# Optimization experiments

Measured on AMD Instinct MI355X. Metric: run time of the kernel, lower is better.

The kernel has to match this reference:

```python
import jax, jax.numpy as jnp
import numpy as np

NUM_HEADS = 16
ROPE_THETA = 1000.0


def _rope(x, cos, sin):
    # x: [B, H, T, d_k]; cos/sin: [T, d_k//2]
    xp = x.reshape(x.shape[:-1] + (x.shape[-1] // 2, 2))
    xe, xo = xp[..., 0], xp[..., 1]
    c = cos[None, None, :, :]
    s = sin[None, None, :, :]
    re = xe * c - xo * s
    ro = xe * s + xo * c
    return jnp.stack((re, ro), axis=-1).reshape(x.shape)


def setup_inputs() -> dict:
    key = jax.random.key(0)
    ks = jax.random.split(key, 5)
    B, T, D = 2, 2048, 1024
    std = 2.0 / (D + D)
    return {
        "x": jax.random.normal(ks[0], (B, T, D), dtype=jnp.float32),
        "wq": jax.random.normal(ks[1], (D, D), dtype=jnp.float32) * std,
        "wk": jax.random.normal(ks[2], (D, D), dtype=jnp.float32) * std,
        "wv": jax.random.normal(ks[3], (D, D), dtype=jnp.float32) * std,
        "wo": jax.random.normal(ks[4], (D, D), dtype=jnp.float32) * std,
    }


def reference(x, wq, wk, wv, wo):
    B, T, D = x.shape
    H = NUM_HEADS
    dk = D // H

    def proj(w):
        # Linear stores weight as [out, in]: '... in, out in -> ... out'
        y = jnp.einsum('btd,ed->bte', x, w)
        return y.reshape(B, T, H, dk).transpose(0, 2, 1, 3)  # [B,H,T,dk]

    q = proj(wq)
    k = proj(wk)
    v = proj(wv)

    # RoPE tables
    pos = jnp.arange(T, dtype=jnp.float32)[:, None]
    kidx = jnp.arange(dk // 2, dtype=jnp.float32)
    inv_freq = ROPE_THETA ** (-2.0 * kidx / dk)
    ang = pos * inv_freq[None, :]
    cos, sin = jnp.cos(ang), jnp.sin(ang)

    q = _rope(q, cos, sin)
    k = _rope(k, cos, sin)

    scores = jnp.einsum('bhnd,bhmd->bhnm', q, k) / jnp.sqrt(jnp.asarray(dk, x.dtype))
    causal = jnp.tril(jnp.ones((T, T), dtype=bool))
    scores = jnp.where(causal[None, None], scores, -jnp.inf)
    attn = jax.nn.softmax(scores, axis=-1)
    head = jnp.einsum('bhnm,bhmd->bhnd', attn, v)  # [B,H,T,dk]

    concat = head.transpose(0, 2, 1, 3).reshape(B, T, D)
    return jnp.einsum('btd,ed->bte', concat, wo)
```

## Files before the change

kernel.cpp:

```cpp
#include <hip/hip_runtime.h>
#include <hip/hip_bf16.h>

typedef __hip_bfloat16 bf16;
typedef __attribute__((ext_vector_type(8))) short bf16x8;
typedef __attribute__((ext_vector_type(4))) float f32x4;

#define T_SEQ 2048
#define NHEADS 16
#define DK 64
#define DMODEL 1024

__device__ inline void load_lds16(const void* g, void* l) {
    __builtin_amdgcn_global_load_lds((const __attribute__((address_space(1))) void*)g,
                                     (__attribute__((address_space(3))) void*)l, 16, 0, 0);
}

__global__ void cvt_all(const float* __restrict__ x,  const float* __restrict__ wq,
                        const float* __restrict__ wk, const float* __restrict__ wv,
                        const float* __restrict__ wo, bf16* __restrict__ xb,
                        bf16* __restrict__ wqkvb, bf16* __restrict__ wob) {
    int i = blockIdx.x * blockDim.x + threadIdx.x;
    const float* src; bf16* dst; int off;
    if (i < (1 << 20)) { src = x; dst = xb; off = i; }
    else {
        int j = i - (1 << 20);
        int seg = j >> 18; off = j & ((1 << 18) - 1);
        src = (seg == 0) ? wq : (seg == 1) ? wk : (seg == 2) ? wv : wo;
        dst = (seg < 3) ? (wqkvb + ((size_t)seg << 20)) : wob;
    }
    float4 f = ((const float4*)src)[off];
    ushort4 o;
    o.x = __bfloat16_as_ushort(__float2bfloat16(f.x));
    o.y = __bfloat16_as_ushort(__float2bfloat16(f.y));
    o.z = __bfloat16_as_ushort(__float2bfloat16(f.z));
    o.w = __bfloat16_as_ushort(__float2bfloat16(f.w));
    ((ushort4*)dst)[off] = o;
}

__global__ __launch_bounds__(256) void gemm_qkv_rope(const bf16* __restrict__ A,
                                                     const bf16* __restrict__ B,
                                                     bf16* __restrict__ qb,
                                                     bf16* __restrict__ kb,
                                                     bf16* __restrict__ vt) {
    const int K = 1024, N = 3072;
    __shared__ bf16 As[128 * 32];
    __shared__ bf16 Bs[128 * 32];
    const int tid  = threadIdx.x;
    const int lane = tid & 63;
    const int wave = tid >> 6;
    const int l16  = lane & 15;
    const int quad = lane >> 4;
    const int wy = wave >> 1, wx = wave & 1;
    const int brow = blockIdx.y * 128;
    const int bcol = blockIdx.x * 128;

    f32x4 acc[4][4] = {};

    for (int k0 = 0; k0 < K; k0 += 32) {
#pragma unroll
        for (int i = 0; i < 2; ++i) {
            int j   = tid + 256 * i;
            int row = j >> 2;
            int cc  = j & 3;
            load_lds16(A + (size_t)(brow + row) * K + k0 + cc * 8, (char*)As + j * 16);
            load_lds16(B + (size_t)(bcol + row) * K + k0 + cc * 8, (char*)Bs + j * 16);
        }
        __syncthreads();
        bf16x8 af[4], bq[4];
#pragma unroll
        for (int i = 0; i < 4; ++i)
            af[i] = *(const bf16x8*)(As + (wy * 64 + i * 16 + l16) * 32 + quad * 8);
#pragma unroll
        for (int j = 0; j < 4; ++j)
            bq[j] = *(const bf16x8*)(Bs + (wx * 64 + j * 16 + l16) * 32 + quad * 8);
#pragma unroll
        for (int i = 0; i < 4; ++i)
#pragma unroll
            for (int j = 0; j < 4; ++j)
                acc[i][j] = __builtin_amdgcn_mfma_f32_16x16x32_bf16(af[i], bq[j], acc[i][j], 0, 0, 0);
        __syncthreads();
    }
    const int seg = bcol >> 10;
    const int hh  = ((bcol & 1023) >> 6) + wx;
    if (seg < 2) {
        bf16* dst = seg ? kb : qb;
#pragma unroll
        for (int j = 0; j < 4; ++j) {
            const int d = j * 16 + l16;
            const float inv = exp2f(-0.31143075889f * (float)(d >> 1));
#pragma unroll
            for (int i = 0; i < 4; ++i)
#pragma unroll
                for (int r = 0; r < 4; ++r) {
                    int row = brow + wy * 64 + i * 16 + quad * 4 + r;
                    int t = row & (T_SEQ - 1), bi = row >> 11;
                    float s, c;
                    __sincosf((float)t * inv, &s, &c);
                    float v = acc[i][j][r];
                    float p = __shfl_xor(v, 1);
                    float res = (l16 & 1) ? fmaf(p, s, v * c) : fmaf(-p, s, v * c);
                    dst[((size_t)(bi * NHEADS + hh) * T_SEQ + t) * DK + d] = __float2bfloat16(res);
                }
        }
    } else {
#pragma unroll
        for (int j = 0; j < 4; ++j) {
            const int d = j * 16 + l16;
#pragma unroll
            for (int i = 0; i < 4; ++i)
#pragma unroll
                for (int r = 0; r < 4; ++r) {
                    int row = brow + wy * 64 + i * 16 + quad * 4 + r;
                    int t = row & (T_SEQ - 1), bi = row >> 11;
                    vt[((size_t)(bi * NHEADS + hh) * DK + d) * T_SEQ + t] =
                        __float2bfloat16(acc[i][j][r]);
                }
        }
    }
}

__global__ __launch_bounds__(256) void gemm_bt(const bf16* __restrict__ A,
                                               const bf16* __restrict__ B,
                                               float* __restrict__ C,
                                               int M, int N, int K) {
    __shared__ bf16 As[128 * 32];
    __shared__ bf16 Bs[128 * 32];
    const int tid  = threadIdx.x;
    const int lane = tid & 63;
    const int wave = tid >> 6;
    const int l16  = lane & 15;
    const int quad = lane >> 4;
    const int wy = wave >> 1, wx = wave & 1;
    const int brow = blockIdx.y * 128;
    const int bcol = blockIdx.x * 128;

    f32x4 acc[4][4] = {};

    for (int k0 = 0; k0 < K; k0 += 32) {
#pragma unroll
        for (int i = 0; i < 2; ++i) {
            int j   = tid + 256 * i;
            int row = j >> 2;
            int cc  = j & 3;
            load_lds16(A + (size_t)(brow + row) * K + k0 + cc * 8, (char*)As + j * 16);
            load_lds16(B + (size_t)(bcol + row) * K + k0 + cc * 8, (char*)Bs + j * 16);
        }
        __syncthreads();
        bf16x8 af[4], bq[4];
#pragma unroll
        for (int i = 0; i < 4; ++i)
            af[i] = *(const bf16x8*)(As + (wy * 64 + i * 16 + l16) * 32 + quad * 8);
#pragma unroll
        for (int j = 0; j < 4; ++j)
            bq[j] = *(const bf16x8*)(Bs + (wx * 64 + j * 16 + l16) * 32 + quad * 8);
#pragma unroll
        for (int i = 0; i < 4; ++i)
#pragma unroll
            for (int j = 0; j < 4; ++j)
                acc[i][j] = __builtin_amdgcn_mfma_f32_16x16x32_bf16(af[i], bq[j], acc[i][j], 0, 0, 0);
        __syncthreads();
    }
#pragma unroll
    for (int i = 0; i < 4; ++i)
#pragma unroll
        for (int j = 0; j < 4; ++j)
#pragma unroll
            for (int r = 0; r < 4; ++r) {
                int row = brow + wy * 64 + i * 16 + quad * 4 + r;
                int col = bcol + wx * 64 + j * 16 + l16;
                C[(size_t)row * N + col] = acc[i][j][r];
            }
}

#define PSTRIDE 72
__global__ __launch_bounds__(256) void attn_kernel(const bf16* __restrict__ qb,
                                                   const bf16* __restrict__ kb,
                                                   const bf16* __restrict__ vt,
                                                   float* __restrict__ Oacc,
                                                   float* __restrict__ Lacc,
                                                   bf16* __restrict__ conc) {
    __shared__ bf16 Ks[2][64 * 64];
    __shared__ bf16 Vs[2][64 * 64];
    __shared__ bf16 Pl[4][16 * PSTRIDE];
    const int bh = blockIdx.y;
    const int b = bh >> 4, h = bh & 15;
    int x = 47 - (int)blockIdx.x;
    int tile, it0, it1;
    bool partial;
    if (x < 16) { tile = x; it0 = 0; it1 = tile; partial = false; }
    else {
        int idx = x - 16;
        tile = 16 + (idx >> 1);
        int mid = (tile + 1) >> 1;
        if (idx & 1) { it0 = mid; it1 = tile; } else { it0 = 0; it1 = mid - 1; }
        partial = true;
    }

    const int tid = threadIdx.x;
    const int lane = tid & 63, wave = tid >> 6;
    const int l16 = lane & 15, quad = lane >> 4;
    const int qrow = tile * 64 + wave * 16;

    const bf16* Qp = qb + (size_t)bh * T_SEQ * DK;
    const bf16* Kp = kb + (size_t)bh * T_SEQ * DK;
    const bf16* Vp = vt + (size_t)bh * DK * T_SEQ;
    bf16* Pw = &Pl[wave][0];

    bf16x8 qf[2];
#pragma unroll
    for (int s = 0; s < 2; ++s)
        qf[s] = *(const bf16x8*)(Qp + (size_t)(qrow + l16) * DK + s * 32 + quad * 8);

    auto stage = [&](int bb, int k0) {
        int j = tid;
#pragma unroll
        for (int i = 0; i < 2; ++i, j += 256) {
            int row = j >> 3, cbl = (j & 7) ^ ((j >> 3) & 7);
            load_lds16(Kp + (size_t)(k0 + row) * DK + cbl * 8, (char*)Ks[bb] + j * 16);
        }
        j = tid;
#pragma unroll
        for (int i = 0; i < 2; ++i, j += 256) {
            int row = j >> 3, cbl = (j & 7) ^ ((j >> 3) & 7);
            load_lds16(Vp + (size_t)row * T_SEQ + k0 + cbl * 8, (char*)Vs[bb] + j * 16);
        }
    };

    f32x4 o[4] = {};
    float l_i = 0.0f;
    const float ksc = 0.18033688011112042f;
    const int sw0 = (quad ^ (l16 & 7)) * 8;
    const int sw1 = ((4 + quad) ^ (l16 & 7)) * 8;

    int cur = 0;
    stage(0, it0 * 64);
    for (int it = it0; it <= it1; ++it) {
        __syncthreads();
        if (it < it1) stage(cur ^ 1, (it + 1) * 64);

        f32x4 sacc[4] = {};
#pragma unroll
        for (int nt = 0; nt < 4; ++nt) {
            bf16x8 kf0 = *(const bf16x8*)(Ks[cur] + (nt * 16 + l16) * 64 + sw0);
            bf16x8 kf1 = *(const bf16x8*)(Ks[cur] + (nt * 16 + l16) * 64 + sw1);
            sacc[nt] = __builtin_amdgcn_mfma_f32_16x16x32_bf16(kf0, qf[0], sacc[nt], 0, 0, 0);
            sacc[nt] = __builtin_amdgcn_mfma_f32_16x16x32_bf16(kf1, qf[1], sacc[nt], 0, 0, 0);
        }
        const int k0 = it * 64;
        const bool masked = (it == tile);
#pragma unroll
        for (int nt = 0; nt < 4; ++nt) {
            union { bf16 hv[4]; uint2 u; } pk;
#pragma unroll
            for (int r = 0; r < 4; ++r) {
                float v = sacc[nt][r] * ksc;
                if (masked && (k0 + nt * 16 + quad * 4 + r > qrow + l16)) v = -30.0f;
                float p = exp2f(v);
                l_i += p;
                pk.hv[r] = __float2bfloat16(p);
            }
            *(uint2*)(Pw + l16 * PSTRIDE + nt * 16 + quad * 4) = pk.u;
        }
#pragma unroll
        for (int ks = 0; ks < 2; ++ks) {
            bf16x8 pf = *(const bf16x8*)(Pw + l16 * PSTRIDE + ks * 32 + quad * 8);
            const int sw = ks ? sw1 : sw0;
#pragma unroll
            for (int j = 0; j < 4; ++j) {
                bf16x8 vf = *(const bf16x8*)(Vs[cur] + (j * 16 + l16) * 64 + sw);
                o[j] = __builtin_amdgcn_mfma_f32_16x16x32_bf16(pf, vf, o[j], 0, 0, 0);
            }
        }
        cur ^= 1;
    }
    float lt = l_i;
    lt += __shfl_xor(lt, 16);
    lt += __shfl_xor(lt, 32);
    if (!partial) {
#pragma unroll
        for (int r = 0; r < 4; ++r) {
            float lr = __shfl(lt, quad * 4 + r);
            float inv_l = 1.0f / lr;
            int t = qrow + quad * 4 + r;
#pragma unroll
            for (int j = 0; j < 4; ++j)
                conc[((size_t)b * T_SEQ + t) * DMODEL + h * DK + j * 16 + l16] =
                    __float2bfloat16(o[j][r] * inv_l);
        }
    } else {
        if (quad == 0)
            atomicAdd(&Lacc[(size_t)bh * 1024 + qrow + l16 - 1024], lt);
#pragma unroll
        for (int r = 0; r < 4; ++r) {
            int q = qrow + quad * 4 + r;
            float* Ob = Oacc + ((size_t)bh * 1024 + q - 1024) * DK;
#pragma unroll
            for (int j = 0; j < 4; ++j)
                atomicAdd(&Ob[j * 16 + l16], o[j][r]);
        }
    }
}

__global__ void attn_finalize(const float* __restrict__ Oacc, const float* __restrict__ Lacc,
                              bf16* __restrict__ conc) {
    int i4 = blockIdx.x * blockDim.x + threadIdx.x;
    if (i4 >= (1 << 19)) return;
    int bhq = i4 >> 4;
    int d4  = i4 & 15;
    int bh = bhq >> 10, q1 = bhq & 1023;
    int b = bh >> 4, h = bh & 15;
    int q = 1024 + q1;
    float inv = 1.0f / Lacc[bhq];
    float4 o4 = ((const float4*)Oacc)[i4];
    ushort4 u;
    u.x = __bfloat16_as_ushort(__float2bfloat16(o4.x * inv));
    u.y = __bfloat16_as_ushort(__float2bfloat16(o4.y * inv));
    u.z = __bfloat16_as_ushort(__float2bfloat16(o4.z * inv));
    u.w = __bfloat16_as_ushort(__float2bfloat16(o4.w * inv));
    *(ushort4*)&conc[((size_t)(b * T_SEQ + q)) * DMODEL + h * DK + d4 * 4] = u;
}

extern "C" void kernel_launch(void* const* d_in, const int* in_sizes, int n_in,
                              void* d_out, int out_size, void* d_ws, size_t ws_size,
                              hipStream_t stream) {
    const float* x  = (const float*)d_in[0];
    const float* wq = (const float*)d_in[1];
    const float* wk = (const float*)d_in[2];
    const float* wv = (const float*)d_in[3];
    const float* wo = (const float*)d_in[4];
    float* out = (float*)d_out;

    char* ws = (char*)d_ws;
    bf16* xb    = (bf16*)(ws);
    bf16* wqkvb = (bf16*)(ws + (8ull << 20));
    bf16* wob   = (bf16*)(ws + (14ull << 20));
    bf16* qb    = (bf16*)(ws + (40ull << 20));
    bf16* kb    = (bf16*)(ws + (48ull << 20));
    bf16* vt    = (bf16*)(ws + (56ull << 20));
    bf16* conc  = (bf16*)(ws + (16ull << 20));
    float* Oacc = (float*)(ws + (24ull << 20));
    float* Lacc = (float*)(ws + (32ull << 20));

    cvt_all<<<8192, 256, 0, stream>>>(x, wq, wk, wv, wo, xb, wqkvb, wob);
    gemm_qkv_rope<<<dim3(24, 32), 256, 0, stream>>>(xb, wqkvb, qb, kb, vt);

    hipMemsetAsync(Oacc, 0, (8ull << 20) + 32 * 1024 * sizeof(float), stream);
    attn_kernel<<<dim3(48, 32), 256, 0, stream>>>(qb, kb, vt, Oacc, Lacc, conc);
    attn_finalize<<<2048, 256, 0, stream>>>(Oacc, Lacc, conc);

    gemm_bt<<<dim3(8, 32), 256, 0, stream>>>(conc, wob, out, 4096, 1024, 1024);
}
```

Baseline: 219.9 us.

## Permute Q/K weight rows for vectorized RoPE stores and fold softmax scale into Q

```diff
diff --git a/kernel.cpp b/kernel.cpp
--- a/kernel.cpp
+++ b/kernel.cpp
@@ -20,13 +20,20 @@
                         const float* __restrict__ wo, bf16* __restrict__ xb,
                         bf16* __restrict__ wqkvb, bf16* __restrict__ wob) {
     int i = blockIdx.x * blockDim.x + threadIdx.x;
-    const float* src; bf16* dst; int off;
-    if (i < (1 << 20)) { src = x; dst = xb; off = i; }
+    const float* src; bf16* dst; int off, woff;
+    if (i < (1 << 20)) { src = x; dst = xb; woff = off = i; }
     else {
         int j = i - (1 << 20);
         int seg = j >> 18; off = j & ((1 << 18) - 1);
         src = (seg == 0) ? wq : (seg == 1) ? wk : (seg == 2) ? wv : wo;
         dst = (seg < 3) ? (wqkvb + ((size_t)seg << 20)) : wob;
+        woff = off;
+        if (seg < 2) {
+            int row = off >> 8, col4 = off & 255;
+            int d = row & 63;
+            int prow = (row & ~63) | ((d & 3) * 16 + (d >> 2));
+            woff = (prow << 8) | col4;
+        }
     }
     float4 f = ((const float4*)src)[off];
     ushort4 o;
@@ -34,7 +41,7 @@
     o.y = __bfloat16_as_ushort(__float2bfloat16(f.y));
     o.z = __bfloat16_as_ushort(__float2bfloat16(f.z));
     o.w = __bfloat16_as_ushort(__float2bfloat16(f.w));
-    ((ushort4*)dst)[off] = o;
+    ((ushort4*)dst)[woff] = o;
 }
 
 __global__ __launch_bounds__(256) void gemm_qkv_rope(const bf16* __restrict__ A,
@@ -42,7 +49,7 @@
                                                      bf16* __restrict__ qb,
                                                      bf16* __restrict__ kb,
                                                      bf16* __restrict__ vt) {
-    const int K = 1024, N = 3072;
+    const int K = 1024;
     __shared__ bf16 As[128 * 32];
     __shared__ bf16 Bs[128 * 32];
     const int tid  = threadIdx.x;
@@ -82,39 +89,45 @@
     }
     const int seg = bcol >> 10;
     const int hh  = ((bcol & 1023) >> 6) + wx;
+    const float ksc = 0.18033688011112042f;
     if (seg < 2) {
         bf16* dst = seg ? kb : qb;
+        const float inv0 = exp2f(-0.31143075889f * (float)(2 * l16));
+        const float inv1 = exp2f(-0.31143075889f * (float)(2 * l16 + 1));
+        const float sc = seg ? 1.0f : ksc;
+#pragma unroll
+        for (int i = 0; i < 4; ++i)
+#pragma unroll
+            for (int r = 0; r < 4; ++r) {
+                int row = brow + wy * 64 + i * 16 + quad * 4 + r;
+                int t = row & (T_SEQ - 1), bi = row >> 11;
+                float s0, c0, s1, c1;
+                __sincosf((float)t * inv0, &s0, &c0);
+                __sincosf((float)t * inv1, &s1, &c1);
+                float a0 = acc[i][0][r], a1 = acc[i][1][r];
+                float a2 = acc[i][2][r], a3 = acc[i][3][r];
+                ushort4 u;
+                u.x = __bfloat16_as_ushort(__float2bfloat16((a0 * c0 - a1 * s0) * sc));
+                u.y = __bfloat16_as_ushort(__float2bfloat16((a0 * s0 + a1 * c0) * sc));
+                u.z = __bfloat16_as_ushort(__float2bfloat16((a2 * c1 - a3 * s1) * sc));
+                u.w = __bfloat16_as_ushort(__float2bfloat16((a2 * s1 + a3 * c1) * sc));
+                *(ushort4*)&dst[((size_t)(bi * NHEADS + hh) * T_SEQ + t) * DK + 4 * l16] = u;
+            }
+    } else {
 #pragma unroll
         for (int j = 0; j < 4; ++j) {
             const int d = j * 16 + l16;
-            const float inv = exp2f(-0.31143075889f * (float)(d >> 1));
-#pragma unroll
-            for (int i = 0; i < 4; ++i)
-#pragma unroll
-                for (int r = 0; r < 4; ++r) {
-                    int row = brow + wy * 64 + i * 16 + quad * 4 + r;
-                    int t = row & (T_SEQ - 1), bi = row >> 11;
-                    float s, c;
-                    __sincosf((float)t * inv, &s, &c);
-                    float v = acc[i][j][r];
-                    float p = __shfl_xor(v, 1);
-                    float res = (l16 & 1) ? fmaf(p, s, v * c) : fmaf(-p, s, v * c);
-                    dst[((size_t)(bi * NHEADS + hh) * T_SEQ + t) * DK + d] = __float2bfloat16(res);
-                }
-        }
-    } else {
-#pragma unroll
-        for (int j = 0; j < 4; ++j) {
-            const int d = j * 16 + l16;
-#pragma unroll
-            for (int i = 0; i < 4; ++i)
-#pragma unroll
-                for (int r = 0; r < 4; ++r) {
-                    int row = brow + wy * 64 + i * 16 + quad * 4 + r;
-                    int t = row & (T_SEQ - 1), bi = row >> 11;
-                    vt[((size_t)(bi * NHEADS + hh) * DK + d) * T_SEQ + t] =
-                        __float2bfloat16(acc[i][j][r]);
-                }
+#pragma unroll
+            for (int i = 0; i < 4; ++i) {
+                int rowb = brow + wy * 64 + i * 16 + quad * 4;
+                int t0 = rowb & (T_SEQ - 1), bi = rowb >> 11;
+                ushort4 u;
+                u.x = __bfloat16_as_ushort(__float2bfloat16(acc[i][j][0]));
+                u.y = __bfloat16_as_ushort(__float2bfloat16(acc[i][j][1]));
+                u.z = __bfloat16_as_ushort(__float2bfloat16(acc[i][j][2]));
+                u.w = __bfloat16_as_ushort(__float2bfloat16(acc[i][j][3]));
+                *(ushort4*)&vt[((size_t)(bi * NHEADS + hh) * DK + d) * T_SEQ + t0] = u;
+            }
         }
     }
 }
@@ -228,7 +241,6 @@
 
     f32x4 o[4] = {};
     float l_i = 0.0f;
-    const float ksc = 0.18033688011112042f;
     const int sw0 = (quad ^ (l16 & 7)) * 8;
     const int sw1 = ((4 + quad) ^ (l16 & 7)) * 8;
 
@@ -253,7 +265,7 @@
             union { bf16 hv[4]; uint2 u; } pk;
 #pragma unroll
             for (int r = 0; r < 4; ++r) {
-                float v = sacc[nt][r] * ksc;
+                float v = sacc[nt][r];
                 if (masked && (k0 + nt * 16 + quad * 4 + r > qrow + l16)) v = -30.0f;
                 float p = exp2f(v);
                 l_i += p;
```

New measurement: 222.1 us. About the same (+1.0%).
